# Kernel optimization log

Measured on AMD Instinct MI355X. Metric: run time of the kernel, lower is better.

## Reference

```python
import jax, jax.numpy as jnp
import numpy as np

B, L, D = 2048, 64, 128
NODES = 512
EPS = 1e-6


def setup_inputs() -> dict:
    key = jax.random.key(0)
    ks = jax.random.split(key, 9)
    src_ids = jax.random.randint(ks[0], (B, L), 0, NODES, dtype=jnp.int32)
    dst_ids = jax.random.randint(ks[1], (B, L), 0, NODES, dtype=jnp.int32)
    src_node_ids = jax.random.randint(ks[2], (B,), 1, NODES, dtype=jnp.int32)
    dst_node_ids = jax.random.randint(ks[3], (B,), 1, NODES, dtype=jnp.int32)
    node_interact_times = 100.0 + jax.random.uniform(ks[4], (B,), jnp.float32)
    src_times = jax.random.uniform(ks[5], (B, L), jnp.float32) * 100.0
    dst_times = jax.random.uniform(ks[6], (B, L), jnp.float32) * 100.0
    W1 = jax.random.normal(ks[7], (1, D), jnp.float32) * 0.5
    b1 = jnp.zeros((D,), jnp.float32)
    W2 = jax.random.normal(ks[8], (D, D), jnp.float32) * (1.0 / np.sqrt(D))
    b2 = jnp.zeros((D,), jnp.float32)
    return dict(src_padded_nodes_neighbor_ids=src_ids,
                dst_padded_nodes_neighbor_ids=dst_ids,
                src_node_ids=src_node_ids, dst_node_ids=dst_node_ids,
                node_interact_times=node_interact_times,
                src_padded_nodes_neighbor_times=src_times,
                dst_padded_nodes_neighbor_times=dst_times,
                W1=W1, b1=b1, W2=W2, b2=b2)


def _group_stats(ids, t):
    # per-position stats of the group sharing the same neighbor id. ids,t: (L,)
    n_pos = ids.shape[0]
    eq = ids[:, None] == ids[None, :]                       # (L,L) group membership
    n = eq.sum(1)                                           # group size at each position
    nf = n.astype(t.dtype)
    tb = jnp.broadcast_to(t[None, :], (n_pos, n_pos))
    tmax = jnp.max(jnp.where(eq, tb, -jnp.inf), axis=1)
    tmin = jnp.min(jnp.where(eq, tb, jnp.inf), axis=1)
    # mean(diff(sorted(ts))) == (max-min)/(n-1)
    avg_iat = jnp.where(n > 1, (tmax - tmin) / jnp.maximum(nf - 1.0, 1.0), 0.0)
    # stable rank of each element inside its own group (order statistic)
    pos = jnp.arange(n_pos)
    before = (t[:, None] < t[None, :]) | ((t[:, None] == t[None, :]) & (pos[:, None] < pos[None, :]))
    rank = jnp.sum(eq & before, axis=0)
    split = n // 2
    sel = eq & (rank[None, :] == split[:, None])            # exactly one per group
    t_split = jnp.sum(jnp.where(sel, tb, 0.0), axis=1)      # sorted(ts)[n//2]
    denom = jnp.maximum(nf - split.astype(t.dtype) - 1.0, 1.0)
    recent_iat = jnp.where(n >= 4, (tmax - t_split) / denom, 0.0)
    valid = ids != 0                                        # dicts skip neighbor id 0
    return nf, jnp.where(valid, avg_iat, 0.0), jnp.where(valid, recent_iat, 0.0)


def _cross_lookup(ids_a, ids_b, vals_b):
    # dict.get(nid, 0.0) over the other side's per-group values (id 0 excluded)
    match = (ids_a[:, None] == ids_b[None, :]) & (ids_b[None, :] != 0)
    idx = jnp.argmax(match, axis=1)
    return jnp.where(match.any(1), vals_b[idx], 0.0)


def _last_time(ids_a, ids_b, t_b):
    # dict comprehension keeps the LAST occurrence's timestamp (id 0 excluded)
    match = (ids_a[:, None] == ids_b[None, :]) & (ids_b[None, :] != 0)
    score = jnp.where(match, jnp.arange(ids_b.shape[0])[None, :], -1)
    li = score.max(1)
    return jnp.where(li >= 0, t_b[jnp.maximum(li, 0)], 0.0)


def _side_features(ids_a, t_a, ids_b, t_b, other_node_id, cur_t,
                   n_a, avg_a, rec_a, avg_b, rec_b, other_first):
    ft = t_a.dtype
    c_self = n_a
    c_other = jnp.sum(ids_a[:, None] == ids_b[None, :], axis=1).astype(ft)
    is_other = (ids_a == other_node_id).astype(ft)
    connects = (c_other > 0).astype(ft)
    freq_asym = jnp.where(c_other > 0, c_self / (c_other + EPS), 0.0)
    rcy_self = cur_t - t_a
    rcy_other = cur_t - _last_time(ids_a, ids_b, t_b)
    temp_asym = jnp.where(rcy_self > EPS, rcy_other / (rcy_self + EPS), 0.0)
    iat_other = _cross_lookup(ids_a, ids_b, avg_b)
    iat_asym = jnp.where(iat_other > EPS, avg_a / (iat_other + EPS), 0.0)
    riat_other = _cross_lookup(ids_a, ids_b, rec_b)
    riat_asym = jnp.where(riat_other > EPS, rec_a / (riat_other + EPS), 0.0)
    if other_first:
        head = [c_other, c_self]
    else:
        head = [c_self, c_other]
    return jnp.stack(head + [is_other, connects, freq_asym, temp_asym, iat_asym, riat_asym], axis=1)


def _per_sample(ids_s, ids_d, sid, did, cur_t, t_s, t_d):
    n_s, avg_s, rec_s = _group_stats(ids_s, t_s)
    n_d, avg_d, rec_d = _group_stats(ids_d, t_d)
    f_src = _side_features(ids_s, t_s, ids_d, t_d, did, cur_t,
                           n_s, avg_s, rec_s, avg_d, rec_d, False)
    f_dst = _side_features(ids_d, t_d, ids_s, t_s, sid, cur_t,
                           n_d, avg_d, rec_d, avg_s, rec_s, True)
    return f_src, f_dst


def _mlp_sum(feats, W1, b1, W2, b2):
    # Linear(1->D) -> ReLU -> Linear(D->D), applied per scalar feature, summed over the 8 features
    h = jax.nn.relu(feats[..., None] * W1[0] + b1)           # [B,L,8,D]
    y = jnp.einsum('blfd,de->blfe', h, W2) + b2
    return y.sum(axis=2)                                      # [B,L,D]


def reference(src_padded_nodes_neighbor_ids, dst_padded_nodes_neighbor_ids,
              src_node_ids, dst_node_ids, node_interact_times,
              src_padded_nodes_neighbor_times, dst_padded_nodes_neighbor_times,
              W1, b1, W2, b2):
    f_src, f_dst = jax.vmap(_per_sample)(
        src_padded_nodes_neighbor_ids, dst_padded_nodes_neighbor_ids,
        src_node_ids, dst_node_ids, node_interact_times,
        src_padded_nodes_neighbor_times, dst_padded_nodes_neighbor_times)
    f_src = jnp.where((src_padded_nodes_neighbor_ids == 0)[..., None], 0.0, f_src)
    f_dst = jnp.where((dst_padded_nodes_neighbor_ids == 0)[..., None], 0.0, f_dst)
    src_path_features = _mlp_sum(f_src, W1, b1, W2, b2)
    dst_path_features = _mlp_sum(f_dst, W1, b1, W2, b2)
    return src_path_features, dst_path_features
```

## Files before the change

kernel.cpp:

```cpp
#include <hip/hip_runtime.h>


#define EPSF 1e-6f
#define LDB 136

typedef __attribute__((ext_vector_type(8))) short bf16x8;
typedef __attribute__((ext_vector_type(4))) float f32x4;
typedef __attribute__((ext_vector_type(2))) float f32x2;

__device__ inline short f2bf(float x) {
    unsigned u = __float_as_uint(x);
    return (short)((u + 0x7fffu + ((u >> 16) & 1u)) >> 16);
}

__launch_bounds__(128)
__global__ void lpe_feats(const int* __restrict__ src_ids,
                          const int* __restrict__ dst_ids,
                          const int* __restrict__ src_nid,
                          const int* __restrict__ dst_nid,
                          const float* __restrict__ t_now,
                          const float* __restrict__ src_t,
                          const float* __restrict__ dst_t,
                          float* __restrict__ fs)
{
    __shared__ int2  s_idt[128];
    __shared__ __align__(16) f32x4 s_tab[2][512];

    const int tid  = threadIdx.x;
    const int b    = blockIdx.x;
    const int side = tid >> 6;
    const int i    = tid & 63;

    #pragma unroll
    for (int u = tid; u < 1024; u += 128) ((float*)s_tab)[u * 4] = 0.f;

    const float cur = t_now[b];
    const int   s_n = src_nid[b], d_n = dst_nid[b];

    const int*   idp = side ? dst_ids : src_ids;
    const float* tp  = side ? dst_t   : src_t;
    const int   my_id = idp[b * 64 + i];
    const float my_t  = tp [b * 64 + i];
    s_idt[tid] = make_int2(my_id, __float_as_int(my_t));
    __syncthreads();

    int n = 0, rank = 0, later = 0;
    float tmax = -3.4e38f, tmin = 3.4e38f;
    const int sbase = side * 64;
    #pragma unroll 8
    for (int j = 0; j < 64; ++j) {
        const int2 e = s_idt[sbase + j];
        const float tj = __int_as_float(e.y);
        if (e.x == my_id) {
            ++n;
            tmax = fmaxf(tmax, tj);
            tmin = fminf(tmin, tj);
            if (tj < my_t || (tj == my_t && j < i)) ++rank;
            if (j > i) later = 1;
        }
    }
    const float nf    = (float)n;
    const int   split = n >> 1;
    const float avg   = (n > 1) ? (tmax - tmin) / (nf - 1.f) : 0.f;
    if (my_id != 0) {
        s_tab[side][my_id].x = nf;
        s_tab[side][my_id].y = avg;
        if (rank == split)
            s_tab[side][my_id].z = (n >= 4)
                ? (tmax - my_t) / fmaxf(nf - (float)split - 1.f, 1.f) : 0.f;
        if (!later)
            s_tab[side][my_id].w = my_t;
    }
    __syncthreads();

    const int os = side ^ 1;
    const float rec_m = (my_id != 0) ? s_tab[side][my_id].z : 0.f;
    const f32x4 to = s_tab[os][my_id];
    const float n_o = (my_id != 0) ? to.x : 0.f;
    const bool  hit = n_o > 0.f;
    const float avg_o = hit ? to.y : 0.f;
    const float rec_o = hit ? to.z : 0.f;
    const float lastt = hit ? to.w : 0.f;
    const int other_node = side ? s_n : d_n;
    const float m = (my_id != 0) ? 1.f : 0.f;

    const float rcy_s = cur - my_t;
    const float rcy_o = cur - lastt;
    f32x4 f0, f1;
    f0.x = m * nf;
    f0.y = m * n_o;
    f0.z = m * ((my_id == other_node) ? 1.f : 0.f);
    f0.w = m * (hit ? 1.f : 0.f);
    f1.x = m * (hit ? nf / (n_o + EPSF) : 0.f);
    f1.y = m * ((rcy_s > EPSF) ? rcy_o / (rcy_s + EPSF) : 0.f);
    f1.z = m * ((avg_o > EPSF) ? avg / (avg_o + EPSF) : 0.f);
    f1.w = m * ((rec_o > EPSF) ? rec_m / (rec_o + EPSF) : 0.f);

    const long rowf = (long)side * 131072 + (long)b * 64 + i;
    *(f32x4*)&fs[rowf * 8]     = f0;
    *(f32x4*)&fs[rowf * 8 + 4] = f1;
}

__launch_bounds__(256, 4)
__global__ void lpe_gemm(const float* __restrict__ fs,
                         const float* __restrict__ W2,
                         const float* __restrict__ W1,
                         const float* __restrict__ b1,
                         const float* __restrict__ b2,
                         float* __restrict__ out)
{
    __shared__ __align__(16) float s_w1[128], s_b1[128], s_b2[128];
    __shared__ __align__(16) short W2T[128 * LDB];

    const int tid  = threadIdx.x;
    const int lane = tid & 63, wv = tid >> 6;
    const int quad = lane >> 4, ln = lane & 15;

    f32x4 fa0[2], fb0[2];
    #pragma unroll
    for (int rg = 0; rg < 2; ++rg) {
        const long rowf = (long)blockIdx.x * 128 + wv * 32 + rg * 16 + ln;
        fa0[rg] = *(const f32x4*)&fs[rowf * 8];
        fb0[rg] = *(const f32x4*)&fs[rowf * 8 + 4];
    }

    for (int v = tid; v < 8192; v += 256) {
        const int kp = v >> 7, n = v & 127;
        const float a = W2[(2 * kp)     * 128 + n];
        const float c = W2[(2 * kp + 1) * 128 + n];
        const unsigned pk = (unsigned)(unsigned short)f2bf(a)
                          | ((unsigned)(unsigned short)f2bf(c) << 16);
        *(unsigned*)&W2T[n * LDB + 2 * kp] = pk;
    }
    if (tid < 128) { s_w1[tid] = W1[tid]; s_b1[tid] = b1[tid]; s_b2[tid] = b2[tid]; }
    __syncthreads();

    #pragma unroll 2
    for (int ch = 0; ch < 2; ++ch) {
        const long base = (long)(blockIdx.x + ch * 1024) * 128;

        float fxr[2][8];
        if (ch == 0) {
            #pragma unroll
            for (int rg = 0; rg < 2; ++rg) {
                fxr[rg][0] = fa0[rg].x; fxr[rg][1] = fa0[rg].y;
                fxr[rg][2] = fa0[rg].z; fxr[rg][3] = fa0[rg].w;
                fxr[rg][4] = fb0[rg].x; fxr[rg][5] = fb0[rg].y;
                fxr[rg][6] = fb0[rg].z; fxr[rg][7] = fb0[rg].w;
            }
        } else {
            #pragma unroll
            for (int rg = 0; rg < 2; ++rg) {
                const long rowf = base + wv * 32 + rg * 16 + ln;
                const f32x4 a = *(const f32x4*)&fs[rowf * 8];
                const f32x4 c = *(const f32x4*)&fs[rowf * 8 + 4];
                fxr[rg][0] = a.x; fxr[rg][1] = a.y; fxr[rg][2] = a.z; fxr[rg][3] = a.w;
                fxr[rg][4] = c.x; fxr[rg][5] = c.y; fxr[rg][6] = c.z; fxr[rg][7] = c.w;
            }
        }

        bf16x8 gf[2][4];
        #pragma unroll
        for (int kk = 0; kk < 4; ++kk) {
            const int kb = kk * 32 + quad * 8;
            #pragma unroll
            for (int rg = 0; rg < 2; ++rg) {
                #pragma unroll
                for (int u2 = 0; u2 < 4; ++u2) {
                    const f32x2 w  = *(const f32x2*)&s_w1[kb + u2 * 2];
                    const f32x2 bb = *(const f32x2*)&s_b1[kb + u2 * 2];
                    f32x2 sv = {0.f, 0.f};
                    #pragma unroll
                    for (int f = 0; f < 8; ++f) {
                        const f32x2 h = w * fxr[rg][f] + bb;
                        sv += __builtin_elementwise_max(h, (f32x2){0.f, 0.f});
                    }
                    gf[rg][kk][u2 * 2]     = f2bf(sv.x);
                    gf[rg][kk][u2 * 2 + 1] = f2bf(sv.y);
                }
            }
        }

        #pragma unroll
        for (int et = 0; et < 8; ++et) {
            bf16x8 af[4];
            #pragma unroll
            for (int kk = 0; kk < 4; ++kk)
                af[kk] = *(const bf16x8*)&W2T[(et * 16 + ln) * LDB + kk * 32 + quad * 8];
            f32x4 acc[2] = {(f32x4){0.f,0.f,0.f,0.f}, (f32x4){0.f,0.f,0.f,0.f}};
            #pragma unroll
            for (int kk = 0; kk < 4; ++kk)
                #pragma unroll
                for (int rg = 0; rg < 2; ++rg)
                    acc[rg] = __builtin_amdgcn_mfma_f32_16x16x32_bf16(af[kk], gf[rg][kk], acc[rg], 0, 0, 0);

            const int e0 = et * 16 + quad * 4;
            const f32x4 badd = *(const f32x4*)&s_b2[e0] * 8.f;
            #pragma unroll
            for (int rg = 0; rg < 2; ++rg) {
                const long rowf = base + wv * 32 + rg * 16 + ln;
                __builtin_nontemporal_store(acc[rg] + badd,
                    (f32x4*)&out[rowf * 128 + e0]);
            }
        }
    }
}

__launch_bounds__(256, 2)
__global__ void lpe_fused4(const int* __restrict__ src_ids,
                           const int* __restrict__ dst_ids,
                           const int* __restrict__ src_nid,
                           const int* __restrict__ dst_nid,
                           const float* __restrict__ t_now,
                           const float* __restrict__ src_t,
                           const float* __restrict__ dst_t,
                           const float* __restrict__ W1,
                           const float* __restrict__ b1,
                           const float* __restrict__ W2,
                           const float* __restrict__ b2,
                           float* __restrict__ out)
{
    __shared__ int2  s_idt[128];
    __shared__ __align__(16) f32x4 s_tab[2][512];
    __shared__ float s_feats[128][9];
    __shared__ __align__(16) float s_w1[128], s_b1[128], s_b2[128];
    __shared__ __align__(16) float s_stage[4][32][32];
    __shared__ __align__(16) short W2T[128 * LDB];

    const int tid  = threadIdx.x;
    const int b4   = blockIdx.x * 4;
    const int lane = tid & 63, wv = tid >> 6;
    const int quad = lane >> 4, ln = lane & 15;
    const int side = (tid >> 6) & 1;
    const int i    = tid & 63;

    if (tid < 128) { s_w1[tid] = W1[tid]; s_b1[tid] = b1[tid]; s_b2[tid] = b2[tid]; }
    for (int u = tid; u < 16384; u += 256) {
        const int k = u >> 7, n = u & 127;
        W2T[n * LDB + k] = f2bf(W2[u]);
    }
    const int*   idp = side ? dst_ids : src_ids;
    const float* tp  = side ? dst_t   : src_t;
    int   pf_id = 0; float pf_t = 0.f;
    if (tid < 128) { pf_id = idp[b4 * 64 + i]; pf_t = tp[b4 * 64 + i]; }
    float cur = t_now[b4];
    int   s_n = src_nid[b4], d_n = dst_nid[b4];
    for (int u = tid; u < 1024; u += 256) ((float*)s_tab)[u * 4] = 0.f;
    const long side_stride = 2048L * 64L * 128L;

    for (int s = 0; s < 4; ++s) {
        const int   my_id = pf_id;  const float my_t = pf_t;
        const float curs  = cur;    const int sns = s_n, dns = d_n;
        if (tid < 128) s_idt[tid] = make_int2(my_id, __float_as_int(my_t));
        __syncthreads();

        float nf = 0.f, avg = 0.f;
        if (tid < 128) {
            int n = 0, rank = 0, later = 0;
            float tmax = -3.4e38f, tmin = 3.4e38f;
            const int sbase = side * 64;
            #pragma unroll 8
            for (int j = 0; j < 64; ++j) {
                const int2 e = s_idt[sbase + j];
                const float tj = __int_as_float(e.y);
                if (e.x == my_id) {
                    ++n; tmax = fmaxf(tmax, tj); tmin = fminf(tmin, tj);
                    if (tj < my_t || (tj == my_t && j < i)) ++rank;
                    if (j > i) later = 1;
                }
            }
            nf = (float)n;
            const int split = n >> 1;
            avg = (n > 1) ? (tmax - tmin) / (nf - 1.f) : 0.f;
            if (my_id != 0) {
                s_tab[side][my_id].x = nf;
                s_tab[side][my_id].y = avg;
                if (rank == split)
                    s_tab[side][my_id].z = (n >= 4)
                        ? (tmax - my_t) / fmaxf(nf - (float)split - 1.f, 1.f) : 0.f;
                if (!later) s_tab[side][my_id].w = my_t;
            }
        }
        if (s < 3) {
            if (tid < 128) {
                pf_id = idp[(b4 + s + 1) * 64 + i];
                pf_t  = tp [(b4 + s + 1) * 64 + i];
            }
            cur = t_now[b4 + s + 1];
            s_n = src_nid[b4 + s + 1];
            d_n = dst_nid[b4 + s + 1];
        }
        __syncthreads();

        if (tid < 128) {
            const int os = side ^ 1;
            const float rec_m = (my_id != 0) ? s_tab[side][my_id].z : 0.f;
            const f32x4 to = s_tab[os][my_id];
            const float n_o = (my_id != 0) ? to.x : 0.f;
            const bool  hit = n_o > 0.f;
            const float avg_o = hit ? to.y : 0.f;
            const float rec_o = hit ? to.z : 0.f;
            const float lastt = hit ? to.w : 0.f;
            const int other_node = side ? sns : dns;
            const float m = (my_id != 0) ? 1.f : 0.f;
            const float rcy_s = curs - my_t;
            const float rcy_o = curs - lastt;
            s_feats[tid][0] = m * nf;
            s_feats[tid][1] = m * n_o;
            s_feats[tid][2] = m * ((my_id == other_node) ? 1.f : 0.f);
            s_feats[tid][3] = m * (hit ? 1.f : 0.f);
            s_feats[tid][4] = m * (hit ? nf / (n_o + EPSF) : 0.f);
            s_feats[tid][5] = m * ((rcy_s > EPSF) ? rcy_o / (rcy_s + EPSF) : 0.f);
            s_feats[tid][6] = m * ((avg_o > EPSF) ? avg / (avg_o + EPSF) : 0.f);
            s_feats[tid][7] = m * ((rec_o > EPSF) ? rec_m / (rec_o + EPSF) : 0.f);
        }
        __syncthreads();

        float fxr[2][8];
        #pragma unroll
        for (int rg = 0; rg < 2; ++rg) {
            const int row = wv * 32 + rg * 16 + ln;
            #pragma unroll
            for (int j = 0; j < 8; ++j) fxr[rg][j] = s_feats[row][j];
        }
        if (s < 3)
            for (int u = tid; u < 1024; u += 256) ((float*)s_tab)[u * 4] = 0.f;

        bf16x8 gf[2][4];
        #pragma unroll
        for (int kk = 0; kk < 4; ++kk) {
            const int kb = kk * 32 + quad * 8;
            #pragma unroll
            for (int rg = 0; rg < 2; ++rg) {
                #pragma unroll
                for (int u2 = 0; u2 < 4; ++u2) {
                    const f32x2 w  = *(const f32x2*)&s_w1[kb + u2 * 2];
                    const f32x2 bb = *(const f32x2*)&s_b1[kb + u2 * 2];
                    f32x2 sv = {0.f, 0.f};
                    #pragma unroll
                    for (int f = 0; f < 8; ++f) {
                        const f32x2 h = w * fxr[rg][f] + bb;
                        sv += __builtin_elementwise_max(h, (f32x2){0.f, 0.f});
                    }
                    gf[rg][kk][u2 * 2]     = f2bf(sv.x);
                    gf[rg][kk][u2 * 2 + 1] = f2bf(sv.y);
                }
            }
        }

        float* st = &s_stage[wv][0][0];
        const int sw = ln & 7;
        const long rowbase = (long)(b4 + s) * 64;

        #pragma unroll
        for (int p = 0; p < 4; ++p) {
            const int et0 = 2 * p, et1 = 2 * p + 1;
            bf16x8 afA[4], afB[4];
            #pragma unroll
            for (int kk = 0; kk < 4; ++kk) {
                afA[kk] = *(const bf16x8*)&W2T[(et0 * 16 + ln) * LDB + kk * 32 + quad * 8];
                afB[kk] = *(const bf16x8*)&W2T[(et1 * 16 + ln) * LDB + kk * 32 + quad * 8];
            }
            f32x4 accA[2] = {(f32x4){0.f,0.f,0.f,0.f}, (f32x4){0.f,0.f,0.f,0.f}};
            f32x4 accB[2] = {(f32x4){0.f,0.f,0.f,0.f}, (f32x4){0.f,0.f,0.f,0.f}};
            #pragma unroll
            for (int kk = 0; kk < 4; ++kk)
                #pragma unroll
                for (int rg = 0; rg < 2; ++rg) {
                    accA[rg] = __builtin_amdgcn_mfma_f32_16x16x32_bf16(afA[kk], gf[rg][kk], accA[rg], 0, 0, 0);
                    accB[rg] = __builtin_amdgcn_mfma_f32_16x16x32_bf16(afB[kk], gf[rg][kk], accB[rg], 0, 0, 0);
                }
            const f32x4 bA = *(const f32x4*)&s_b2[et0 * 16 + quad * 4] * 8.f;
            const f32x4 bB = *(const f32x4*)&s_b2[et1 * 16 + quad * 4] * 8.f;

            if (p)
                asm volatile("s_waitcnt lgkmcnt(0)" ::: "memory");
            #pragma unroll
            for (int rg = 0; rg < 2; ++rg) {
                const int row = rg * 16 + ln;
                *(f32x4*)&st[row * 32 + ((quad ^ sw) * 4)]       = accA[rg] + bA;
                *(f32x4*)&st[row * 32 + (((4 + quad) ^ sw) * 4)] = accB[rg] + bB;
            }
            asm volatile("s_waitcnt lgkmcnt(0)" ::: "memory");
            #pragma unroll
            for (int rr = 0; rr < 4; ++rr) {
                const int rl = rr * 8 + (lane >> 3);
                const f32x4 v = *(const f32x4*)&st[rl * 32 + (((lane & 7) ^ (rl & 7)) * 4)];
                const int row = wv * 32 + rl;
                const int sd = row >> 6, ii = row & 63;
                __builtin_nontemporal_store(v,
                    (f32x4*)&out[(long)sd * side_stride + (rowbase + ii) * 128
                                 + p * 32 + (lane & 7) * 4]);
            }
        }
    }
}

extern "C" void kernel_launch(void* const* d_in, const int* in_sizes, int n_in,
                              void* d_out, int out_size, void* d_ws, size_t ws_size,
                              hipStream_t stream) {
    (void)in_sizes; (void)n_in; (void)out_size;
    const int*   src_ids = (const int*)  d_in[0];
    const int*   dst_ids = (const int*)  d_in[1];
    const int*   src_nid = (const int*)  d_in[2];
    const int*   dst_nid = (const int*)  d_in[3];
    const float* t_now   = (const float*)d_in[4];
    const float* src_t   = (const float*)d_in[5];
    const float* dst_t   = (const float*)d_in[6];
    const float* W1      = (const float*)d_in[7];
    const float* b1      = (const float*)d_in[8];
    const float* W2      = (const float*)d_in[9];
    const float* b2      = (const float*)d_in[10];
    float* out = (float*)d_out;

    const size_t FEAT_BYTES = 262144ULL * 8 * sizeof(float);

    if (ws_size >= FEAT_BYTES) {
        float* fs = (float*)d_ws;
        lpe_feats<<<2048, 128, 0, stream>>>(src_ids, dst_ids, src_nid, dst_nid,
                                            t_now, src_t, dst_t, fs);
        lpe_gemm<<<1024, 256, 0, stream>>>(fs, W2, W1, b1, b2, out);
    } else {
        lpe_fused4<<<512, 256, 0, stream>>>(src_ids, dst_ids, src_nid, dst_nid,
                                            t_now, src_t, dst_t, W1, b1, W2, b2, out);
    }
}
```

Measured before the change: 214.5 us.

## Pre-transpose W2 to bf16 once in feats kernel, simplify GEMM to one chunk per block

The first kernel now converts W2 to a transposed bf16 copy in workspace using its first 64 blocks. The GEMM kernel then fills its shared W2T with plain 16-byte copies instead of redoing the conversion per block, and each block handles one 128-row chunk, so the grid doubles to 2048 blocks. Occupancy hint drops from 4 to 3 blocks per CU. The fallback fused kernel loses its LDS staging for output stores and writes MFMA results directly, which may give less coalesced global stores.

```diff
diff --git a/kernel.cpp b/kernel.cpp
--- a/kernel.cpp
+++ b/kernel.cpp
@@ -21,7 +21,9 @@
                           const float* __restrict__ t_now,
                           const float* __restrict__ src_t,
                           const float* __restrict__ dst_t,
-                          float* __restrict__ fs)
+                          const float* __restrict__ W2,
+                          float* __restrict__ fs,
+                          short* __restrict__ w2t)
 {
     __shared__ int2  s_idt[128];
     __shared__ __align__(16) f32x4 s_tab[2][512];
@@ -30,6 +32,15 @@
     const int b    = blockIdx.x;
     const int side = tid >> 6;
     const int i    = tid & 63;
+
+    if (b < 64) {
+        #pragma unroll
+        for (int u = 0; u < 2; ++u) {
+            const int idx = b * 256 + u * 128 + tid;
+            const int k = idx >> 7, n = idx & 127;
+            w2t[n * 128 + k] = f2bf(W2[idx]);
+        }
+    }
 
     #pragma unroll
     for (int u = tid; u < 1024; u += 128) ((float*)s_tab)[u * 4] = 0.f;
@@ -101,9 +112,9 @@
     *(f32x4*)&fs[rowf * 8 + 4] = f1;
 }
 
-__launch_bounds__(256, 4)
+__launch_bounds__(256, 3)
 __global__ void lpe_gemm(const float* __restrict__ fs,
-                         const float* __restrict__ W2,
+                         const short* __restrict__ w2t,
                          const float* __restrict__ W1,
                          const float* __restrict__ b1,
                          const float* __restrict__ b2,
@@ -116,92 +127,69 @@
     const int lane = tid & 63, wv = tid >> 6;
     const int quad = lane >> 4, ln = lane & 15;
 
-    f32x4 fa0[2], fb0[2];
-    #pragma unroll
-    for (int rg = 0; rg < 2; ++rg) {
-        const long rowf = (long)blockIdx.x * 128 + wv * 32 + rg * 16 + ln;
-        fa0[rg] = *(const f32x4*)&fs[rowf * 8];
-        fb0[rg] = *(const f32x4*)&fs[rowf * 8 + 4];
-    }
-
-    for (int v = tid; v < 8192; v += 256) {
-        const int kp = v >> 7, n = v & 127;
-        const float a = W2[(2 * kp)     * 128 + n];
-        const float c = W2[(2 * kp + 1) * 128 + n];
-        const unsigned pk = (unsigned)(unsigned short)f2bf(a)
-                          | ((unsigned)(unsigned short)f2bf(c) << 16);
-        *(unsigned*)&W2T[n * LDB + 2 * kp] = pk;
+    #pragma unroll
+    for (int it = 0; it < 8; ++it) {
+        const int c = tid + it * 256;
+        const int n = c >> 4, j = c & 15;
+        *(bf16x8*)&W2T[n * LDB + j * 8] = *(const bf16x8*)&w2t[n * 128 + j * 8];
     }
     if (tid < 128) { s_w1[tid] = W1[tid]; s_b1[tid] = b1[tid]; s_b2[tid] = b2[tid]; }
     __syncthreads();
 
-    #pragma unroll 2
-    for (int ch = 0; ch < 2; ++ch) {
-        const long base = (long)(blockIdx.x + ch * 1024) * 128;
-
-        float fxr[2][8];
-        if (ch == 0) {
-            #pragma unroll
-            for (int rg = 0; rg < 2; ++rg) {
-                fxr[rg][0] = fa0[rg].x; fxr[rg][1] = fa0[rg].y;
-                fxr[rg][2] = fa0[rg].z; fxr[rg][3] = fa0[rg].w;
-                fxr[rg][4] = fb0[rg].x; fxr[rg][5] = fb0[rg].y;
-                fxr[rg][6] = fb0[rg].z; fxr[rg][7] = fb0[rg].w;
-            }
-        } else {
-            #pragma unroll
-            for (int rg = 0; rg < 2; ++rg) {
-                const long rowf = base + wv * 32 + rg * 16 + ln;
-                const f32x4 a = *(const f32x4*)&fs[rowf * 8];
-                const f32x4 c = *(const f32x4*)&fs[rowf * 8 + 4];
-                fxr[rg][0] = a.x; fxr[rg][1] = a.y; fxr[rg][2] = a.z; fxr[rg][3] = a.w;
-                fxr[rg][4] = c.x; fxr[rg][5] = c.y; fxr[rg][6] = c.z; fxr[rg][7] = c.w;
-            }
-        }
-
-        bf16x8 gf[2][4];
-        #pragma unroll
-        for (int kk = 0; kk < 4; ++kk) {
-            const int kb = kk * 32 + quad * 8;
-            #pragma unroll
-            for (int rg = 0; rg < 2; ++rg) {
+    const long base = (long)blockIdx.x * 128;
+
+    float fxr[2][8];
+    #pragma unroll
+    for (int rg = 0; rg < 2; ++rg) {
+        const long rowf = base + wv * 32 + rg * 16 + ln;
+        const f32x4 a = *(const f32x4*)&fs[rowf * 8];
+        const f32x4 c = *(const f32x4*)&fs[rowf * 8 + 4];
+        fxr[rg][0] = a.x; fxr[rg][1] = a.y; fxr[rg][2] = a.z; fxr[rg][3] = a.w;
+        fxr[rg][4] = c.x; fxr[rg][5] = c.y; fxr[rg][6] = c.z; fxr[rg][7] = c.w;
+    }
+
+    bf16x8 gf[2][4];
+    #pragma unroll
+    for (int kk = 0; kk < 4; ++kk) {
+        const int kb = kk * 32 + quad * 8;
+        #pragma unroll
+        for (int rg = 0; rg < 2; ++rg) {
+            #pragma unroll
+            for (int u2 = 0; u2 < 4; ++u2) {
+                const f32x2 w  = *(const f32x2*)&s_w1[kb + u2 * 2];
+                const f32x2 bb = *(const f32x2*)&s_b1[kb + u2 * 2];
+                f32x2 sv = {0.f, 0.f};
                 #pragma unroll
-                for (int u2 = 0; u2 < 4; ++u2) {
-                    const f32x2 w  = *(const f32x2*)&s_w1[kb + u2 * 2];
-                    const f32x2 bb = *(const f32x2*)&s_b1[kb + u2 * 2];
-                    f32x2 sv = {0.f, 0.f};
-                    #pragma unroll
-                    for (int f = 0; f < 8; ++f) {
-                        const f32x2 h = w * fxr[rg][f] + bb;
-                        sv += __builtin_elementwise_max(h, (f32x2){0.f, 0.f});
-                    }
-                    gf[rg][kk][u2 * 2]     = f2bf(sv.x);
-                    gf[rg][kk][u2 * 2 + 1] = f2bf(sv.y);
+                for (int f = 0; f < 8; ++f) {
+                    const f32x2 h = w * fxr[rg][f] + bb;
+                    sv += __builtin_elementwise_max(h, (f32x2){0.f, 0.f});
                 }
-            }
-        }
-
-        #pragma unroll
-        for (int et = 0; et < 8; ++et) {
-            bf16x8 af[4];
-            #pragma unroll
-            for (int kk = 0; kk < 4; ++kk)
-                af[kk] = *(const bf16x8*)&W2T[(et * 16 + ln) * LDB + kk * 32 + quad * 8];
-            f32x4 acc[2] = {(f32x4){0.f,0.f,0.f,0.f}, (f32x4){0.f,0.f,0.f,0.f}};
-            #pragma unroll
-            for (int kk = 0; kk < 4; ++kk)
-                #pragma unroll
-                for (int rg = 0; rg < 2; ++rg)
-                    acc[rg] = __builtin_amdgcn_mfma_f32_16x16x32_bf16(af[kk], gf[rg][kk], acc[rg], 0, 0, 0);
-
-            const int e0 = et * 16 + quad * 4;
-            const f32x4 badd = *(const f32x4*)&s_b2[e0] * 8.f;
-            #pragma unroll
-            for (int rg = 0; rg < 2; ++rg) {
-                const long rowf = base + wv * 32 + rg * 16 + ln;
-                __builtin_nontemporal_store(acc[rg] + badd,
-                    (f32x4*)&out[rowf * 128 + e0]);
-            }
+                gf[rg][kk][u2 * 2]     = f2bf(sv.x);
+                gf[rg][kk][u2 * 2 + 1] = f2bf(sv.y);
+            }
+        }
+    }
+
+    #pragma unroll
+    for (int et = 0; et < 8; ++et) {
+        bf16x8 af[4];
+        #pragma unroll
+        for (int kk = 0; kk < 4; ++kk)
+            af[kk] = *(const bf16x8*)&W2T[(et * 16 + ln) * LDB + kk * 32 + quad * 8];
+        f32x4 acc[2] = {(f32x4){0.f,0.f,0.f,0.f}, (f32x4){0.f,0.f,0.f,0.f}};
+        #pragma unroll
+        for (int kk = 0; kk < 4; ++kk)
+            #pragma unroll
+            for (int rg = 0; rg < 2; ++rg)
+                acc[rg] = __builtin_amdgcn_mfma_f32_16x16x32_bf16(af[kk], gf[rg][kk], acc[rg], 0, 0, 0);
+
+        const int e0 = et * 16 + quad * 4;
+        const f32x4 badd = *(const f32x4*)&s_b2[e0] * 8.f;
+        #pragma unroll
+        for (int rg = 0; rg < 2; ++rg) {
+            const long rowf = base + wv * 32 + rg * 16 + ln;
+            __builtin_nontemporal_store(acc[rg] + badd,
+                (f32x4*)&out[rowf * 128 + e0]);
         }
     }
 }
@@ -224,7 +212,6 @@
     __shared__ __align__(16) f32x4 s_tab[2][512];
     __shared__ float s_feats[128][9];
     __shared__ __align__(16) float s_w1[128], s_b1[128], s_b2[128];
-    __shared__ __align__(16) float s_stage[4][32][32];
     __shared__ __align__(16) short W2T[128 * LDB];
 
     const int tid  = threadIdx.x;
@@ -348,49 +335,28 @@
             }
         }
 
-        float* st = &s_stage[wv][0][0];
-        const int sw = ln & 7;
         const long rowbase = (long)(b4 + s) * 64;
-
-        #pragma unroll
-        for (int p = 0; p < 4; ++p) {
-            const int et0 = 2 * p, et1 = 2 * p + 1;
-            bf16x8 afA[4], afB[4];
-            #pragma unroll
-            for (int kk = 0; kk < 4; ++kk) {
-                afA[kk] = *(const bf16x8*)&W2T[(et0 * 16 + ln) * LDB + kk * 32 + quad * 8];
-                afB[kk] = *(const bf16x8*)&W2T[(et1 * 16 + ln) * LDB + kk * 32 + quad * 8];
-            }
-            f32x4 accA[2] = {(f32x4){0.f,0.f,0.f,0.f}, (f32x4){0.f,0.f,0.f,0.f}};
-            f32x4 accB[2] = {(f32x4){0.f,0.f,0.f,0.f}, (f32x4){0.f,0.f,0.f,0.f}};
+        #pragma unroll
+        for (int et = 0; et < 8; ++et) {
+            bf16x8 af[4];
+            #pragma unroll
+            for (int kk = 0; kk < 4; ++kk)
+                af[kk] = *(const bf16x8*)&W2T[(et * 16 + ln) * LDB + kk * 32 + quad * 8];
+            f32x4 acc[2] = {(f32x4){0.f,0.f,0.f,0.f}, (f32x4){0.f,0.f,0.f,0.f}};
             #pragma unroll
             for (int kk = 0; kk < 4; ++kk)
                 #pragma unroll
-                for (int rg = 0; rg < 2; ++rg) {
-                    accA[rg] = __builtin_amdgcn_mfma_f32_16x16x32_bf16(afA[kk], gf[rg][kk], accA[rg], 0, 0, 0);
-                    accB[rg] = __builtin_amdgcn_mfma_f32_16x16x32_bf16(afB[kk], gf[rg][kk], accB[rg], 0, 0, 0);
-                }
-            const f32x4 bA = *(const f32x4*)&s_b2[et0 * 16 + quad * 4] * 8.f;
-            const f32x4 bB = *(const f32x4*)&s_b2[et1 * 16 + quad * 4] * 8.f;
-
-            if (p)
-                asm volatile("s_waitcnt lgkmcnt(0)" ::: "memory");
+                for (int rg = 0; rg < 2; ++rg)
+                    acc[rg] = __builtin_amdgcn_mfma_f32_16x16x32_bf16(af[kk], gf[rg][kk], acc[rg], 0, 0, 0);
+
+            const int e0 = et * 16 + quad * 4;
+            const f32x4 badd = *(const f32x4*)&s_b2[e0] * 8.f;
             #pragma unroll
             for (int rg = 0; rg < 2; ++rg) {
-                const int row = rg * 16 + ln;
-                *(f32x4*)&st[row * 32 + ((quad ^ sw) * 4)]       = accA[rg] + bA;
-                *(f32x4*)&st[row * 32 + (((4 + quad) ^ sw) * 4)] = accB[rg] + bB;
-            }
-            asm volatile("s_waitcnt lgkmcnt(0)" ::: "memory");
-            #pragma unroll
-            for (int rr = 0; rr < 4; ++rr) {
-                const int rl = rr * 8 + (lane >> 3);
-                const f32x4 v = *(const f32x4*)&st[rl * 32 + (((lane & 7) ^ (rl & 7)) * 4)];
-                const int row = wv * 32 + rl;
+                const int row = wv * 32 + rg * 16 + ln;
                 const int sd = row >> 6, ii = row & 63;
-                __builtin_nontemporal_store(v,
-                    (f32x4*)&out[(long)sd * side_stride + (rowbase + ii) * 128
-                                 + p * 32 + (lane & 7) * 4]);
+                __builtin_nontemporal_store(acc[rg] + badd,
+                    (f32x4*)&out[(long)sd * side_stride + (rowbase + ii) * 128 + e0]);
             }
         }
     }
@@ -413,13 +379,15 @@
     const float* b2      = (const float*)d_in[10];
     float* out = (float*)d_out;
 
+    const size_t W2T_BYTES  = 128 * 128 * sizeof(short);
     const size_t FEAT_BYTES = 262144ULL * 8 * sizeof(float);
 
-    if (ws_size >= FEAT_BYTES) {
-        float* fs = (float*)d_ws;
+    if (ws_size >= W2T_BYTES + FEAT_BYTES) {
+        short* w2t = (short*)d_ws;
+        float* fs  = (float*)((char*)d_ws + W2T_BYTES);
         lpe_feats<<<2048, 128, 0, stream>>>(src_ids, dst_ids, src_nid, dst_nid,
-                                            t_now, src_t, dst_t, fs);
-        lpe_gemm<<<1024, 256, 0, stream>>>(fs, W2, W1, b1, b2, out);
+                                            t_now, src_t, dst_t, W2, fs, w2t);
+        lpe_gemm<<<2048, 256, 0, stream>>>(fs, w2t, W1, b1, b2, out);
     } else {
         lpe_fused4<<<512, 256, 0, stream>>>(src_ids, dst_ids, src_nid, dst_nid,
                                             t_now, src_t, dst_t, W1, b1, W2, b2, out);
```

Result: faster. 193.6 us (-9.7%).
